# Kernel optimization log

Hardware: AMD Instinct MI355X
Metric: run time of the kernel (lower is better)

## Reference

```python
import jax, jax.numpy as jnp
import numpy as np

B, S, D, H, F = 2, 2048, 1024, 16, 4096
DH = D // H  # per-head dim = 64
EPS = 1e-5


def _layer_norm(x, g, b):
    mu = jnp.mean(x, axis=-1, keepdims=True)
    var = jnp.mean((x - mu) ** 2, axis=-1, keepdims=True)
    return (x - mu) * jax.lax.rsqrt(var + EPS) * g + b


def _mha(q_in, kv_in, wq, bq, wk, bk, wv, bv, wo, bo, causal):
    b, s, d = q_in.shape
    q = (q_in @ wq + bq).reshape(b, s, H, DH).transpose(0, 2, 1, 3)
    k = (kv_in @ wk + bk).reshape(b, s, H, DH).transpose(0, 2, 1, 3)
    v = (kv_in @ wv + bv).reshape(b, s, H, DH).transpose(0, 2, 1, 3)
    scores = jnp.einsum('bhqd,bhkd->bhqk', q, k) / np.sqrt(DH).astype(np.float32)
    if causal:
        mask = jnp.tril(jnp.ones((s, s), dtype=bool))
        scores = jnp.where(mask, scores, -jnp.inf)
    attn = jax.nn.softmax(scores, axis=-1)
    out = jnp.einsum('bhqk,bhkd->bhqd', attn, v)
    out = out.transpose(0, 2, 1, 3).reshape(b, s, d)
    return out @ wo + bo


def setup_inputs() -> dict:
    key = jax.random.key(0)
    ks = iter(jax.random.split(key, 24))
    def w(shape, fan_in):
        return jax.random.normal(next(ks), shape, jnp.float32) / np.sqrt(fan_in).astype(np.float32)
    inp = {
        'encoder_output': jax.random.normal(next(ks), (B, S, D), jnp.float32),
        'decoder_input': jax.random.normal(next(ks), (B, S, D), jnp.float32),
    }
    for pre in ('sa', 'ca'):
        for nm in ('wq', 'wk', 'wv', 'wo'):
            inp[f'{pre}_{nm}'] = w((D, D), D)
            inp[f'{pre}_b{nm[-1]}'] = jnp.zeros((D,), jnp.float32)
        inp[f'{pre}_g'] = jnp.ones((D,), jnp.float32)
        inp[f'{pre}_bt'] = jnp.zeros((D,), jnp.float32)
    inp['f_w1'] = w((D, F), D); inp['f_b1'] = jnp.zeros((F,), jnp.float32)
    inp['f_w2'] = w((F, D), F); inp['f_b2'] = jnp.zeros((D,), jnp.float32)
    inp['f_g'] = jnp.ones((D,), jnp.float32); inp['f_bt'] = jnp.zeros((D,), jnp.float32)
    return inp


def reference(encoder_output, decoder_input,
              sa_wq, sa_bq, sa_wk, sa_bk, sa_wv, sa_bv, sa_wo, sa_bo, sa_g, sa_bt,
              ca_wq, ca_bq, ca_wk, ca_bk, ca_wv, ca_bv, ca_wo, ca_bo, ca_g, ca_bt,
              f_w1, f_b1, f_w2, f_b2, f_g, f_bt):
    # masked self-attention + residual + LN
    x = _mha(decoder_input, decoder_input, sa_wq, sa_bq, sa_wk, sa_bk, sa_wv, sa_bv, sa_wo, sa_bo, True)
    x = _layer_norm(x + decoder_input, sa_g, sa_bt)
    # encoder-decoder attention + residual + LN
    y = _mha(x, encoder_output, ca_wq, ca_bq, ca_wk, ca_bk, ca_wv, ca_bv, ca_wo, ca_bo, False)
    y = _layer_norm(y + x, ca_g, ca_bt)
    # FFN + residual + LN
    h = jax.nn.relu(y @ f_w1 + f_b1) @ f_w2 + f_b2
    return _layer_norm(h + y, f_g, f_bt)
```

## Files before the change

### kernel.cpp

```cpp
#include <hip/hip_runtime.h>
#include <hip/hip_bf16.h>


typedef __attribute__((ext_vector_type(8))) short bf16x8;
typedef __attribute__((ext_vector_type(4))) float f32x4;

#define LOG2E 1.44269504088896340736f

constexpr int Bb = 2, Ss = 2048, Dd = 1024, Hh = 16, DHd = 64, Ff = 4096;
constexpr int Mrows = Bb * Ss;
constexpr int BHS = Bb * Hh * Ss;

static __device__ __forceinline__ ushort f2b(float f) {
    union { float f; unsigned u; } x{f};
    unsigned r = x.u + 0x7fffu + ((x.u >> 16) & 1u);
    return (ushort)(r >> 16);
}

static __device__ __forceinline__ unsigned pk2(float a, float b) {
    __hip_bfloat162 h = __float22bfloat162_rn(make_float2(a, b));
    unsigned u;
    __builtin_memcpy(&u, &h, 4);
    return u;
}

static __device__ __forceinline__ unsigned pk2t(float a, float b) {
    union { float f; unsigned u; } ua{a}, ub{b};
    return __builtin_amdgcn_perm(ub.u, ua.u, 0x07060302);
}

static __device__ __forceinline__ void gl2lds16(const void* g, void* l) {
    __builtin_amdgcn_global_load_lds(
        (const __attribute__((address_space(1))) void*)g,
        (__attribute__((address_space(3))) void*)l, 16, 0, 0);
}

__global__ __launch_bounds__(256) void cvt_kernel(const float* __restrict__ in,
                                                  ushort* __restrict__ out) {
    int i = (blockIdx.x * 256 + threadIdx.x) * 4;
    float4 v = *(const float4*)(in + i);
    ushort4 u;
    u.x = f2b(v.x); u.y = f2b(v.y); u.z = f2b(v.z); u.w = f2b(v.w);
    *(ushort4*)(out + i) = u;
}

__global__ __launch_bounds__(256) void wtrans_kernel(const float* __restrict__ w,
                                                     ushort* __restrict__ wT,
                                                     int K, int N) {
    __shared__ float t[32][33];
    int tx = threadIdx.x & 31, ty = threadIdx.x >> 5;
    int kb = blockIdx.y * 32, nb = blockIdx.x * 32;
#pragma unroll
    for (int i = 0; i < 4; i++)
        t[ty + i * 8][tx] = w[(size_t)(kb + ty + i * 8) * N + nb + tx];
    __syncthreads();
#pragma unroll
    for (int i = 0; i < 4; i++)
        wT[(size_t)(nb + ty + i * 8) * K + kb + tx] = f2b(t[tx][ty + i * 8]);
}

__global__ __launch_bounds__(256) void pack_bias(const float* __restrict__ a,
                                                 const float* __restrict__ b,
                                                 const float* __restrict__ c,
                                                 float* __restrict__ out) {
    int i = blockIdx.x * 256 + threadIdx.x;
    const float* src = a; int j = i;
    if (i >= 2048)      { src = c; j = i - 2048; }
    else if (i >= 1024) { src = b; j = i - 1024; }
    out[i] = src[j];
}

__global__ __launch_bounds__(256) void gemm_kernel(const ushort* __restrict__ A,
                                                   const ushort* __restrict__ BT,
                                                   const float* __restrict__ bias,
                                                   void* __restrict__ out,
                                                   int M, int N, int K, int klen,
                                                   int mode, int relu, float qsc,
                                                   int vwhich) {
    __shared__ __align__(16) ushort As[128 * 64];
    __shared__ __align__(16) ushort Bs[128 * 64];
    const int tid = threadIdx.x;
    const int lane = tid & 63, wave = tid >> 6;
    const int lr = lane & 15, quad = lane >> 4;
    const int wm = wave & 1, wn = wave >> 1;
    const int m0 = blockIdx.y * 128, n0 = blockIdx.x * 128;
    const int kz = blockIdx.z;
    const int kstart = kz * klen;

    f32x4 acc[4][4];
#pragma unroll
    for (int i = 0; i < 4; i++)
#pragma unroll
        for (int j = 0; j < 4; j++) acc[i][j] = (f32x4){0.f, 0.f, 0.f, 0.f};

    const int srow = tid >> 3;
    const int gchunk = ((tid & 7) ^ (srow & 7)) * 8;
    const ushort* aBase = A + (size_t)(m0 + srow) * K + gchunk;
    const ushort* bBase = BT + (size_t)(n0 + srow) * K + gchunk;
    const size_t rowStep = (size_t)32 * K;

    const int slotA = ((quad) ^ (lr & 7)) * 8;
    const int slotB = ((4 + quad) ^ (lr & 7)) * 8;

    for (int k0 = kstart; k0 < kstart + klen; k0 += 64) {
#pragma unroll
        for (int c = 0; c < 4; c++) {
            gl2lds16(aBase + c * rowStep + k0, &As[c * 2048 + tid * 8]);
            gl2lds16(bBase + c * rowStep + k0, &Bs[c * 2048 + tid * 8]);
        }
        __syncthreads();
#pragma unroll
        for (int kk = 0; kk < 2; kk++) {
            const int slot = kk ? slotB : slotA;
            bf16x8 af[4], bfr[4];
#pragma unroll
            for (int i = 0; i < 4; i++)
                af[i] = *(const bf16x8*)&As[(wm * 64 + i * 16 + lr) * 64 + slot];
#pragma unroll
            for (int j = 0; j < 4; j++)
                bfr[j] = *(const bf16x8*)&Bs[(wn * 64 + j * 16 + lr) * 64 + slot];
#pragma unroll
            for (int i = 0; i < 4; i++)
#pragma unroll
                for (int j = 0; j < 4; j++)
                    acc[i][j] = __builtin_amdgcn_mfma_f32_16x16x32_bf16(af[i], bfr[j], acc[i][j], 0, 0, 0);
        }
        __syncthreads();
    }

#pragma unroll
    for (int j = 0; j < 4; j++) {
        int col = n0 + wn * 64 + j * 16 + lr;
        float bv = (bias && kz == 0) ? bias[col] : 0.f;
#pragma unroll
        for (int i = 0; i < 4; i++) {
            int row0 = m0 + wm * 64 + i * 16 + quad * 4;
            float v[4];
#pragma unroll
            for (int r = 0; r < 4; r++) {
                v[r] = acc[i][j][r] + bv;
                if (relu) v[r] = fmaxf(v[r], 0.f);
            }
            if (mode == 0) {
                float* op = (float*)out + (size_t)kz * M * N;
#pragma unroll
                for (int r = 0; r < 4; r++)
                    op[(size_t)(row0 + r) * N + col] = v[r];
            } else if (mode == 1) {
#pragma unroll
                for (int r = 0; r < 4; r++)
                    ((ushort*)out)[(size_t)(row0 + r) * N + col] = f2b(v[r]);
            } else {
                int which = col >> 10, n1 = col & 1023;
                int h = n1 >> 6, dh = n1 & 63;
                int b = row0 >> 11, s0 = row0 & 2047;
                size_t wbase = (size_t)which * (Bb * Hh * Ss * DHd);
                if (which == vwhich) {
                    uint2 pk;
                    pk.x = pk2(v[0], v[1]); pk.y = pk2(v[2], v[3]);
                    *(uint2*)((ushort*)out + wbase +
                              ((size_t)(b * Hh + h) * DHd + dh) * Ss + s0) = pk;
                } else {
                    float sc = (which == 0) ? qsc : 1.f;
#pragma unroll
                    for (int r = 0; r < 4; r++)
                        ((ushort*)out)[wbase + (((size_t)(b * Hh + h) * Ss + s0 + r) * DHd) + dh] =
                            f2b(v[r] * sc);
                }
            }
        }
    }
}

__global__ __launch_bounds__(256, 5) void attn_kernel(const ushort* __restrict__ Q,
                                                      const ushort* __restrict__ Kg,
                                                      const ushort* __restrict__ VT,
                                                      float* __restrict__ Op0,
                                                      float* __restrict__ Op1,
                                                      float* __restrict__ Ml,
                                                      int causal) {
    __shared__ ushort Ks[64][72];
    __shared__ ushort Vs[64][72];
    __shared__ ushort Ps[4][16][72];
    const int tid = threadIdx.x;
    const int lane = tid & 63, w = tid >> 6;
    const int lr = lane & 15, quad = lane >> 4;
    const int p = blockIdx.z;
    const int qt = causal ? (gridDim.x - 1 - blockIdx.x) : blockIdx.x;
    const int bh = blockIdx.y;
    const size_t hb = (size_t)bh * Ss * DHd;
    const int qrow = qt * 64 + w * 16;
    const int qg = qrow + lr;

    bf16x8 qf0 = *(const bf16x8*)(Q + hb + (size_t)qg * DHd + quad * 8);
    bf16x8 qf1 = *(const bf16x8*)(Q + hb + (size_t)qg * DHd + 32 + quad * 8);

    f32x4 o[4];
#pragma unroll
    for (int d = 0; d < 4; d++) o[d] = (f32x4){0.f, 0.f, 0.f, 0.f};
    float l_i = 0.f;

    const int srow = tid >> 3, sseg = tid & 7;

    const int ktEnd = causal ? (qt + 1) : (Ss / 64);
    for (int kt = p; kt < ktEnd; kt += 2) {
        const int k0 = kt * 64;
#pragma unroll
        for (int io = 0; io < 2; io++) {
            *(bf16x8*)&Ks[srow + io * 32][sseg * 8] =
                *(const bf16x8*)(Kg + hb + (size_t)(k0 + srow + io * 32) * DHd + sseg * 8);
            *(bf16x8*)&Vs[srow + io * 32][sseg * 8] =
                *(const bf16x8*)(VT + hb + (size_t)(srow + io * 32) * Ss + k0 + sseg * 8);
        }
        __syncthreads();

        f32x4 st[4];
#pragma unroll
        for (int k16 = 0; k16 < 4; k16++) {
            bf16x8 a0 = *(const bf16x8*)&Ks[k16 * 16 + lr][quad * 8];
            bf16x8 a1 = *(const bf16x8*)&Ks[k16 * 16 + lr][32 + quad * 8];
            f32x4 z = (f32x4){0.f, 0.f, 0.f, 0.f};
            z = __builtin_amdgcn_mfma_f32_16x16x32_bf16(a0, qf0, z, 0, 0, 0);
            st[k16] = __builtin_amdgcn_mfma_f32_16x16x32_bf16(a1, qf1, z, 0, 0, 0);
        }
        if (causal && kt == qt) {
#pragma unroll
            for (int k16 = 0; k16 < 4; k16++)
#pragma unroll
                for (int r = 0; r < 4; r++) {
                    int key = k0 + k16 * 16 + quad * 4 + r;
                    if (key > qg) st[k16][r] = -1e30f;
                }
        }
        float pv[4][4], psum = 0.f;
#pragma unroll
        for (int k16 = 0; k16 < 4; k16++)
#pragma unroll
            for (int r = 0; r < 4; r++) {
                pv[k16][r] = __builtin_amdgcn_exp2f(fminf(st[k16][r], 88.f));
                psum += pv[k16][r];
            }
        psum += __shfl_xor(psum, 16);
        psum += __shfl_xor(psum, 32);
        l_i += psum;
#pragma unroll
        for (int k16 = 0; k16 < 4; k16++) {
            uint2 pk;
            pk.x = pk2t(pv[k16][0], pv[k16][1]);
            pk.y = pk2t(pv[k16][2], pv[k16][3]);
            *(uint2*)&Ps[w][lr][k16 * 16 + quad * 4] = pk;
        }
#pragma unroll
        for (int kh = 0; kh < 2; kh++) {
            bf16x8 pb = *(const bf16x8*)&Ps[w][lr][kh * 32 + quad * 8];
#pragma unroll
            for (int dt = 0; dt < 4; dt++) {
                bf16x8 av = *(const bf16x8*)&Vs[dt * 16 + lr][kh * 32 + quad * 8];
                o[dt] = __builtin_amdgcn_mfma_f32_16x16x32_bf16(av, pb, o[dt], 0, 0, 0);
            }
        }
        __syncthreads();
    }

    float* Op = p ? Op1 : Op0;
    if (quad == 0)
        Ml[(size_t)p * BHS + (size_t)bh * Ss + qg] = l_i;
    size_t ob = ((size_t)bh * Ss + qg) * 64;
#pragma unroll
    for (int dt = 0; dt < 4; dt++)
        *(f32x4*)(Op + ob + dt * 16 + quad * 4) = o[dt];
}

__global__ __launch_bounds__(256) void attn_combine(const float* __restrict__ Op0,
                                                    const float* __restrict__ Op1,
                                                    const float* __restrict__ Ml,
                                                    ushort* __restrict__ O) {
    int g = blockIdx.x * 256 + threadIdx.x;
    int q = g >> 4, seg = g & 15;
    float inv = 1.f / (Ml[q] + Ml[BHS + q]);
    f32x4 x = *(const f32x4*)(Op0 + (size_t)q * 64 + seg * 4);
    f32x4 y = *(const f32x4*)(Op1 + (size_t)q * 64 + seg * 4);
    int bh = q >> 11, sq = q & 2047, bb = bh >> 4, h = bh & 15;
    uint2 u;
    u.x = pk2((x[0] + y[0]) * inv, (x[1] + y[1]) * inv);
    u.y = pk2((x[2] + y[2]) * inv, (x[3] + y[3]) * inv);
    *(uint2*)(O + ((size_t)(bb * Ss + sq)) * Dd + h * 64 + seg * 4) = u;
}

__global__ __launch_bounds__(256) void ln_kernel(const float* __restrict__ a0,
                                                 const float* __restrict__ a1,
                                                 const float* __restrict__ a2,
                                                 const float* __restrict__ a3,
                                                 const float* __restrict__ resid,
                                                 const float* __restrict__ g,
                                                 const float* __restrict__ bt,
                                                 float* __restrict__ out32,
                                                 ushort* __restrict__ outb) {
    const int row = blockIdx.x, tid = threadIdx.x;
    const size_t base = (size_t)row * Dd + tid * 4;
    float4 av = *(const float4*)(a0 + base);
    if (a1) { float4 t = *(const float4*)(a1 + base); av.x += t.x; av.y += t.y; av.z += t.z; av.w += t.w; }
    if (a2) { float4 t = *(const float4*)(a2 + base); av.x += t.x; av.y += t.y; av.z += t.z; av.w += t.w; }
    if (a3) { float4 t = *(const float4*)(a3 + base); av.x += t.x; av.y += t.y; av.z += t.z; av.w += t.w; }
    float4 rv = *(const float4*)(resid + base);
    float x0 = av.x + rv.x, x1 = av.y + rv.y, x2 = av.z + rv.z, x3 = av.w + rv.w;
    float s = x0 + x1 + x2 + x3;
    float q = x0 * x0 + x1 * x1 + x2 * x2 + x3 * x3;
#pragma unroll
    for (int off = 1; off <= 32; off <<= 1) {
        s += __shfl_xor(s, off);
        q += __shfl_xor(q, off);
    }
    __shared__ float red[8];
    int wave = tid >> 6, lane = tid & 63;
    if (lane == 0) { red[wave] = s; red[4 + wave] = q; }
    __syncthreads();
    s = red[0] + red[1] + red[2] + red[3];
    q = red[4] + red[5] + red[6] + red[7];
    float mu = s * (1.f / Dd);
    float var = q * (1.f / Dd) - mu * mu;
    float rs = rsqrtf(var + 1e-5f);
    int col = tid * 4;
    float4 gv = *(const float4*)(g + col);
    float4 bv = *(const float4*)(bt + col);
    float y0 = (x0 - mu) * rs * gv.x + bv.x;
    float y1 = (x1 - mu) * rs * gv.y + bv.y;
    float y2 = (x2 - mu) * rs * gv.z + bv.z;
    float y3 = (x3 - mu) * rs * gv.w + bv.w;
    if (out32) *(float4*)(out32 + base) = make_float4(y0, y1, y2, y3);
    if (outb) {
        ushort4 u; u.x = f2b(y0); u.y = f2b(y1); u.z = f2b(y2); u.w = f2b(y3);
        *(ushort4*)(outb + base) = u;
    }
}

constexpr size_t OFF_XB     = 0;
constexpr size_t OFF_ENCB   = OFF_XB     + 8388608;
constexpr size_t OFF_QKVWT  = OFF_ENCB   + 8388608;
constexpr size_t OFF_CAWQT  = OFF_QKVWT  + 6291456;
constexpr size_t OFF_CAKVT  = OFF_CAWQT  + 2097152;
constexpr size_t OFF_SAWOT  = OFF_CAKVT  + 4194304;
constexpr size_t OFF_CAWOT  = OFF_SAWOT  + 2097152;
constexpr size_t OFF_FW1T   = OFF_CAWOT  + 2097152;
constexpr size_t OFF_FW2T   = OFF_FW1T   + 8388608;
constexpr size_t OFF_SABQKV = OFF_FW2T   + 8388608;
constexpr size_t OFF_CABKV  = OFF_SABQKV + 12288;
constexpr size_t OFF_QB     = OFF_CABKV  + 8192;
constexpr size_t OFF_KB     = OFF_QB     + 8388608;
constexpr size_t OFF_VB     = OFF_KB     + 8388608;
constexpr size_t OFF_ATTNO  = OFF_VB     + 8388608;
constexpr size_t OFF_F1     = OFF_ATTNO  + 8388608;
constexpr size_t OFF_F2     = OFF_F1     + 16777216;
constexpr size_t OFF_X1B    = OFF_F2     + 16777216;
constexpr size_t OFF_F3     = OFF_X1B    + 8388608;
constexpr size_t OFF_YB     = OFF_F3     + 16777216;
constexpr size_t OFF_H1B    = OFF_YB     + 8388608;

extern "C" void kernel_launch(void* const* d_in, const int* in_sizes, int n_in,
                              void* d_out, int out_size, void* d_ws, size_t ws_size,
                              hipStream_t stream) {
    const float* enc   = (const float*)d_in[0];
    const float* dec   = (const float*)d_in[1];
    const float* sa_wq = (const float*)d_in[2];
    const float* sa_bq = (const float*)d_in[3];
    const float* sa_wk = (const float*)d_in[4];
    const float* sa_bk = (const float*)d_in[5];
    const float* sa_wv = (const float*)d_in[6];
    const float* sa_bv = (const float*)d_in[7];
    const float* sa_wo = (const float*)d_in[8];
    const float* sa_bo = (const float*)d_in[9];
    const float* sa_g  = (const float*)d_in[10];
    const float* sa_bt = (const float*)d_in[11];
    const float* ca_wq = (const float*)d_in[12];
    const float* ca_bq = (const float*)d_in[13];
    const float* ca_wk = (const float*)d_in[14];
    const float* ca_bk = (const float*)d_in[15];
    const float* ca_wv = (const float*)d_in[16];
    const float* ca_bv = (const float*)d_in[17];
    const float* ca_wo = (const float*)d_in[18];
    const float* ca_bo = (const float*)d_in[19];
    const float* ca_g  = (const float*)d_in[20];
    const float* ca_bt = (const float*)d_in[21];
    const float* f_w1  = (const float*)d_in[22];
    const float* f_b1  = (const float*)d_in[23];
    const float* f_w2  = (const float*)d_in[24];
    const float* f_b2  = (const float*)d_in[25];
    const float* f_g   = (const float*)d_in[26];
    const float* f_bt  = (const float*)d_in[27];

    char* ws = (char*)d_ws;
    ushort* xb     = (ushort*)(ws + OFF_XB);
    ushort* encb   = (ushort*)(ws + OFF_ENCB);
    ushort* qkvwT  = (ushort*)(ws + OFF_QKVWT);
    ushort* cawqT  = (ushort*)(ws + OFF_CAWQT);
    ushort* cakvT  = (ushort*)(ws + OFF_CAKVT);
    ushort* sawoT  = (ushort*)(ws + OFF_SAWOT);
    ushort* cawoT  = (ushort*)(ws + OFF_CAWOT);
    ushort* fw1T   = (ushort*)(ws + OFF_FW1T);
    ushort* fw2T   = (ushort*)(ws + OFF_FW2T);
    float*  sabqkv = (float*)(ws + OFF_SABQKV);
    float*  cabkv  = (float*)(ws + OFF_CABKV);
    ushort* qb     = (ushort*)(ws + OFF_QB);
    ushort* kb     = (ushort*)(ws + OFF_KB);
    ushort* vbt    = (ushort*)(ws + OFF_VB);
    ushort* attno  = (ushort*)(ws + OFF_ATTNO);
    float*  f1     = (float*)(ws + OFF_F1);
    float*  f2     = (float*)(ws + OFF_F2);
    ushort* x1b    = (ushort*)(ws + OFF_X1B);
    float*  x1f    = (float*)(ws + OFF_F3);
    ushort* yb     = (ushort*)(ws + OFF_YB);
    ushort* h1b    = (ushort*)(ws + OFF_H1B);
    float*  yfp    = (float*)(ws + OFF_QB);
    float*  ml     = (float*)(ws + OFF_H1B);

    const float QSC = 0.125f * LOG2E;
    const size_t MN = (size_t)Mrows * Dd;

    cvt_kernel<<<4096, 256, 0, stream>>>(dec, xb);
    cvt_kernel<<<4096, 256, 0, stream>>>(enc, encb);
    dim3 tgDD(32, 32);
    wtrans_kernel<<<tgDD, 256, 0, stream>>>(sa_wq, qkvwT,                 Dd, Dd);
    wtrans_kernel<<<tgDD, 256, 0, stream>>>(sa_wk, qkvwT + 1024 * 1024,   Dd, Dd);
    wtrans_kernel<<<tgDD, 256, 0, stream>>>(sa_wv, qkvwT + 2 * 1024 * 1024, Dd, Dd);
    wtrans_kernel<<<tgDD, 256, 0, stream>>>(sa_wo, sawoT,                 Dd, Dd);
    wtrans_kernel<<<tgDD, 256, 0, stream>>>(ca_wq, cawqT,                 Dd, Dd);
    wtrans_kernel<<<tgDD, 256, 0, stream>>>(ca_wk, cakvT,                 Dd, Dd);
    wtrans_kernel<<<tgDD, 256, 0, stream>>>(ca_wv, cakvT + 1024 * 1024,   Dd, Dd);
    wtrans_kernel<<<tgDD, 256, 0, stream>>>(ca_wo, cawoT,                 Dd, Dd);
    wtrans_kernel<<<dim3(128, 32), 256, 0, stream>>>(f_w1, fw1T, Dd, Ff);
    wtrans_kernel<<<dim3(32, 128), 256, 0, stream>>>(f_w2, fw2T, Ff, Dd);
    pack_bias<<<12, 256, 0, stream>>>(sa_bq, sa_bk, sa_bv, sabqkv);
    pack_bias<<<8, 256, 0, stream>>>(ca_bk, ca_bv, nullptr, cabkv);

    gemm_kernel<<<dim3(24, 32, 1), 256, 0, stream>>>(xb, qkvwT, sabqkv, qb,
                                                     Mrows, 3072, Dd, Dd, 2, 0, QSC, 2);
    attn_kernel<<<dim3(32, 32, 2), 256, 0, stream>>>(qb, kb, vbt, f1, x1f, ml, 1);
    attn_combine<<<4096, 256, 0, stream>>>(f1, x1f, ml, attno);
    gemm_kernel<<<dim3(8, 32, 2), 256, 0, stream>>>(attno, sawoT, sa_bo, f1,
                                                    Mrows, Dd, Dd, 512, 0, 0, 1.f, -1);
    ln_kernel<<<4096, 256, 0, stream>>>(f1, f2, nullptr, nullptr, dec,
                                        sa_g, sa_bt, x1f, x1b);

    gemm_kernel<<<dim3(8, 32, 1), 256, 0, stream>>>(x1b, cawqT, ca_bq, qb,
                                                    Mrows, Dd, Dd, Dd, 2, 0, QSC, -1);
    gemm_kernel<<<dim3(16, 32, 1), 256, 0, stream>>>(encb, cakvT, cabkv, kb,
                                                     Mrows, 2048, Dd, Dd, 2, 0, 1.f, 1);
    attn_kernel<<<dim3(32, 32, 2), 256, 0, stream>>>(qb, kb, vbt, f1, f2, ml, 0);
    attn_combine<<<4096, 256, 0, stream>>>(f1, f2, ml, attno);
    gemm_kernel<<<dim3(8, 32, 2), 256, 0, stream>>>(attno, cawoT, ca_bo, f1,
                                                    Mrows, Dd, Dd, 512, 0, 0, 1.f, -1);
    ln_kernel<<<4096, 256, 0, stream>>>(f1, f2, nullptr, nullptr, x1f,
                                        ca_g, ca_bt, yfp, yb);

    gemm_kernel<<<dim3(32, 32, 1), 256, 0, stream>>>(yb, fw1T, f_b1, h1b,
                                                     Mrows, Ff, Dd, Dd, 1, 1, 1.f, -1);
    gemm_kernel<<<dim3(8, 32, 4), 256, 0, stream>>>(h1b, fw2T, f_b2, f1,
                                                    Mrows, Dd, Ff, 1024, 0, 0, 1.f, -1);
    ln_kernel<<<4096, 256, 0, stream>>>(f1, f1 + MN, f1 + 2 * MN, f1 + 3 * MN, yfp,
                                        f_g, f_bt, (float*)d_out, nullptr);
}
```

Baseline: 639.6 us.

## Use 32x32 MFMA with 128-row query tiles and register-resident P in attention

Attention now uses 32x32x16 bf16 MFMA with each wave owning 32 query rows, so a block covers 128 queries and every K/V tile loaded into shared memory is reused across twice as many queries. The softmax probabilities stay in registers and are rearranged into B-operand fragments with cross-half lane shuffles, which removes the per-wave Ps shared-memory round trip. The grid is halved to match. The cost is more registers (launch bounds occupancy lowered from 5 to 4), fewer blocks in flight, and coarser causal tiles that compute more masked work on the diagonal.

```diff
diff --git a/kernel.cpp b/kernel.cpp
--- a/kernel.cpp
+++ b/kernel.cpp
@@ -4,6 +4,7 @@
 
 typedef __attribute__((ext_vector_type(8))) short bf16x8;
 typedef __attribute__((ext_vector_type(4))) float f32x4;
+typedef __attribute__((ext_vector_type(16))) float f32x16;
 
 #define LOG2E 1.44269504088896340736f
 
@@ -172,7 +173,7 @@
     }
 }
 
-__global__ __launch_bounds__(256, 5) void attn_kernel(const ushort* __restrict__ Q,
+__global__ __launch_bounds__(256, 4) void attn_kernel(const ushort* __restrict__ Q,
                                                       const ushort* __restrict__ Kg,
                                                       const ushort* __restrict__ VT,
                                                       float* __restrict__ Op0,
@@ -181,28 +182,31 @@
                                                       int causal) {
     __shared__ ushort Ks[64][72];
     __shared__ ushort Vs[64][72];
-    __shared__ ushort Ps[4][16][72];
     const int tid = threadIdx.x;
     const int lane = tid & 63, w = tid >> 6;
-    const int lr = lane & 15, quad = lane >> 4;
+    const int l31 = lane & 31, h = lane >> 5;
     const int p = blockIdx.z;
     const int qt = causal ? (gridDim.x - 1 - blockIdx.x) : blockIdx.x;
     const int bh = blockIdx.y;
     const size_t hb = (size_t)bh * Ss * DHd;
-    const int qrow = qt * 64 + w * 16;
-    const int qg = qrow + lr;
-
-    bf16x8 qf0 = *(const bf16x8*)(Q + hb + (size_t)qg * DHd + quad * 8);
-    bf16x8 qf1 = *(const bf16x8*)(Q + hb + (size_t)qg * DHd + 32 + quad * 8);
-
-    f32x4 o[4];
-#pragma unroll
-    for (int d = 0; d < 4; d++) o[d] = (f32x4){0.f, 0.f, 0.f, 0.f};
+    const int qrow = qt * 128 + w * 32;
+    const int qg = qrow + l31;
+
+    bf16x8 qf[4];
+#pragma unroll
+    for (int m = 0; m < 4; m++)
+        qf[m] = *(const bf16x8*)(Q + hb + (size_t)qg * DHd + m * 16 + h * 8);
+
+    f32x16 o[2];
+#pragma unroll
+    for (int dt = 0; dt < 2; dt++)
+#pragma unroll
+        for (int r = 0; r < 16; r++) o[dt][r] = 0.f;
     float l_i = 0.f;
 
     const int srow = tid >> 3, sseg = tid & 7;
 
-    const int ktEnd = causal ? (qt + 1) : (Ss / 64);
+    const int ktEnd = causal ? (2 * qt + 2) : (Ss / 64);
     for (int kt = p; kt < ktEnd; kt += 2) {
         const int k0 = kt * 64;
 #pragma unroll
@@ -214,61 +218,77 @@
         }
         __syncthreads();
 
-        f32x4 st[4];
-#pragma unroll
-        for (int k16 = 0; k16 < 4; k16++) {
-            bf16x8 a0 = *(const bf16x8*)&Ks[k16 * 16 + lr][quad * 8];
-            bf16x8 a1 = *(const bf16x8*)&Ks[k16 * 16 + lr][32 + quad * 8];
-            f32x4 z = (f32x4){0.f, 0.f, 0.f, 0.f};
-            z = __builtin_amdgcn_mfma_f32_16x16x32_bf16(a0, qf0, z, 0, 0, 0);
-            st[k16] = __builtin_amdgcn_mfma_f32_16x16x32_bf16(a1, qf1, z, 0, 0, 0);
-        }
-        if (causal && kt == qt) {
-#pragma unroll
-            for (int k16 = 0; k16 < 4; k16++)
-#pragma unroll
-                for (int r = 0; r < 4; r++) {
-                    int key = k0 + k16 * 16 + quad * 4 + r;
-                    if (key > qg) st[k16][r] = -1e30f;
+        float psum = 0.f;
+        unsigned P[2][8];
+#pragma unroll
+        for (int kh = 0; kh < 2; kh++) {
+            f32x16 st;
+#pragma unroll
+            for (int r = 0; r < 16; r++) st[r] = 0.f;
+#pragma unroll
+            for (int m = 0; m < 4; m++) {
+                bf16x8 a = *(const bf16x8*)&Ks[kh * 32 + l31][m * 16 + h * 8];
+                st = __builtin_amdgcn_mfma_f32_32x32x16_bf16(a, qf[m], st, 0, 0, 0);
+            }
+            if (causal && kt >= 2 * qt) {
+#pragma unroll
+                for (int r = 0; r < 16; r++) {
+                    int key = k0 + kh * 32 + (r & 3) + 8 * (r >> 2) + 4 * h;
+                    if (key > qg) st[r] = -1e30f;
                 }
-        }
-        float pv[4][4], psum = 0.f;
-#pragma unroll
-        for (int k16 = 0; k16 < 4; k16++)
-#pragma unroll
-            for (int r = 0; r < 4; r++) {
-                pv[k16][r] = __builtin_amdgcn_exp2f(fminf(st[k16][r], 88.f));
-                psum += pv[k16][r];
-            }
-        psum += __shfl_xor(psum, 16);
+            }
+            float pv[16];
+#pragma unroll
+            for (int r = 0; r < 16; r++) {
+                pv[r] = __builtin_amdgcn_exp2f(fminf(st[r], 88.f));
+                psum += pv[r];
+            }
+#pragma unroll
+            for (int i = 0; i < 8; i++) P[kh][i] = pk2t(pv[2 * i], pv[2 * i + 1]);
+        }
         psum += __shfl_xor(psum, 32);
         l_i += psum;
-#pragma unroll
-        for (int k16 = 0; k16 < 4; k16++) {
-            uint2 pk;
-            pk.x = pk2t(pv[k16][0], pv[k16][1]);
-            pk.y = pk2t(pv[k16][2], pv[k16][3]);
-            *(uint2*)&Ps[w][lr][k16 * 16 + quad * 4] = pk;
-        }
-#pragma unroll
-        for (int kh = 0; kh < 2; kh++) {
-            bf16x8 pb = *(const bf16x8*)&Ps[w][lr][kh * 32 + quad * 8];
-#pragma unroll
-            for (int dt = 0; dt < 4; dt++) {
-                bf16x8 av = *(const bf16x8*)&Vs[dt * 16 + lr][kh * 32 + quad * 8];
-                o[dt] = __builtin_amdgcn_mfma_f32_16x16x32_bf16(av, pb, o[dt], 0, 0, 0);
-            }
-        }
+
+        bf16x8 bfrag[4];
+#pragma unroll
+        for (int kh = 0; kh < 2; kh++)
+#pragma unroll
+            for (int mm = 0; mm < 2; mm++) {
+                int sbase = 2 * (2 * mm + 1 - h);
+                unsigned s0 = P[kh][sbase], s1 = P[kh][sbase + 1];
+                unsigned r0 = __shfl_xor(s0, 32), r1 = __shfl_xor(s1, 32);
+                int lbase = 4 * mm + 2 * h;
+                union { unsigned u[4]; bf16x8 v; } bu;
+                if (h == 0) {
+                    bu.u[0] = P[kh][lbase]; bu.u[1] = P[kh][lbase + 1];
+                    bu.u[2] = r0;           bu.u[3] = r1;
+                } else {
+                    bu.u[0] = r0;           bu.u[1] = r1;
+                    bu.u[2] = P[kh][lbase]; bu.u[3] = P[kh][lbase + 1];
+                }
+                bfrag[kh * 2 + mm] = bu.v;
+            }
+#pragma unroll
+        for (int dt = 0; dt < 2; dt++)
+#pragma unroll
+            for (int m = 0; m < 4; m++) {
+                bf16x8 a = *(const bf16x8*)&Vs[dt * 32 + l31][m * 16 + h * 8];
+                o[dt] = __builtin_amdgcn_mfma_f32_32x32x16_bf16(a, bfrag[m], o[dt], 0, 0, 0);
+            }
         __syncthreads();
     }
 
     float* Op = p ? Op1 : Op0;
-    if (quad == 0)
+    if (h == 0)
         Ml[(size_t)p * BHS + (size_t)bh * Ss + qg] = l_i;
     size_t ob = ((size_t)bh * Ss + qg) * 64;
 #pragma unroll
-    for (int dt = 0; dt < 4; dt++)
-        *(f32x4*)(Op + ob + dt * 16 + quad * 4) = o[dt];
+    for (int dt = 0; dt < 2; dt++)
+#pragma unroll
+        for (int g = 0; g < 4; g++) {
+            f32x4 v = {o[dt][4 * g], o[dt][4 * g + 1], o[dt][4 * g + 2], o[dt][4 * g + 3]};
+            *(f32x4*)(Op + ob + dt * 32 + g * 8 + 4 * h) = v;
+        }
 }
 
 __global__ __launch_bounds__(256) void attn_combine(const float* __restrict__ Op0,
@@ -434,7 +454,7 @@
 
     gemm_kernel<<<dim3(24, 32, 1), 256, 0, stream>>>(xb, qkvwT, sabqkv, qb,
                                                      Mrows, 3072, Dd, Dd, 2, 0, QSC, 2);
-    attn_kernel<<<dim3(32, 32, 2), 256, 0, stream>>>(qb, kb, vbt, f1, x1f, ml, 1);
+    attn_kernel<<<dim3(16, 32, 2), 256, 0, stream>>>(qb, kb, vbt, f1, x1f, ml, 1);
     attn_combine<<<4096, 256, 0, stream>>>(f1, x1f, ml, attno);
     gemm_kernel<<<dim3(8, 32, 2), 256, 0, stream>>>(attno, sawoT, sa_bo, f1,
                                                     Mrows, Dd, Dd, 512, 0, 0, 1.f, -1);
@@ -445,7 +465,7 @@
                                                     Mrows, Dd, Dd, Dd, 2, 0, QSC, -1);
     gemm_kernel<<<dim3(16, 32, 1), 256, 0, stream>>>(encb, cakvT, cabkv, kb,
                                                      Mrows, 2048, Dd, Dd, 2, 0, 1.f, 1);
-    attn_kernel<<<dim3(32, 32, 2), 256, 0, stream>>>(qb, kb, vbt, f1, f2, ml, 0);
+    attn_kernel<<<dim3(16, 32, 2), 256, 0, stream>>>(qb, kb, vbt, f1, f2, ml, 0);
     attn_combine<<<4096, 256, 0, stream>>>(f1, f2, ml, attno);
     gemm_kernel<<<dim3(8, 32, 2), 256, 0, stream>>>(attno, cawoT, ca_bo, f1,
                                                     Mrows, Dd, Dd, 512, 0, 0, 1.f, -1);
```

Measured after the change: 671.9 us. +5.1%, slower.
